# Kernel optimization log

Hardware: AMD Instinct MI355X
Metric: run time of the kernel (lower is better)

## Reference

```python
import jax, jax.numpy as jnp
import numpy as np

B, N, D_IN, D_OUT, H = 8, 1024, 768, 768, 12
D_HEAD = D_OUT // H  # 64; per-head softmax scale is sqrt(D_HEAD)


def setup_inputs() -> dict:
    key = jax.random.key(0)
    kx, kq, kk, kv, kwo, kbo = jax.random.split(key, 6)
    s_in = 1.0 / np.sqrt(D_IN)
    s_out = 1.0 / np.sqrt(D_OUT)
    return {
        "x": jax.random.normal(kx, (B, N, D_IN), dtype=jnp.float32),
        # stacked per-head Linear weights, torch layout [out, in] -> [H, d_head, D_IN]
        "Wq": jax.random.uniform(kq, (H, D_HEAD, D_IN), jnp.float32, -s_in, s_in),
        "Wk": jax.random.uniform(kk, (H, D_HEAD, D_IN), jnp.float32, -s_in, s_in),
        "Wv": jax.random.uniform(kv, (H, D_HEAD, D_IN), jnp.float32, -s_in, s_in),
        "Wo": jax.random.uniform(kwo, (D_OUT, D_OUT), jnp.float32, -s_out, s_out),
        "bo": jax.random.uniform(kbo, (D_OUT,), jnp.float32, -s_out, s_out),
    }


def reference(x, Wq, Wk, Wv, Wo, bo):
    # Per-head projections, batched over heads: [B, H, N, d_head]
    q = jnp.einsum('bnd,hed->bhne', x, Wq)
    k = jnp.einsum('bnd,hed->bhne', x, Wk)
    v = jnp.einsum('bnd,hed->bhne', x, Wv)
    scale = 1.0 / np.sqrt(D_HEAD)
    scores = jnp.einsum('bhie,bhje->bhij', q, k) * scale  # [B, H, N, N]
    att = jax.nn.softmax(scores, axis=-1)
    out = jnp.einsum('bhij,bhje->bhie', att, v)  # [B, H, N, d_head]
    # concat heads along last dim: [B, N, H*d_head]
    out = out.transpose(0, 2, 1, 3).reshape(B, N, D_OUT)
    return out @ Wo.T + bo
```

## Files before the change

kernel.cpp:

```cpp
#include <hip/hip_runtime.h>
#include <hip/hip_bf16.h>


typedef unsigned short u16;
typedef unsigned int u32;
typedef __attribute__((ext_vector_type(8))) short bf8;
typedef __attribute__((ext_vector_type(4))) short bf4;
typedef __attribute__((ext_vector_type(4))) float f4;
typedef __attribute__((ext_vector_type(4))) unsigned short us4;

#define NB 8
#define NSEQ 1024
#define DMODEL 768
#define NHEAD 12
#define DHEAD 64

#define XELEMS   (NB * NSEQ * DMODEL)
#define WELEMS   (DMODEL * DMODEL)

__device__ __forceinline__ float b2f(u16 u) {
  union { unsigned int i; float f; } c; c.i = ((unsigned int)u) << 16; return c.f;
}
__device__ __forceinline__ u16 f2b(float f) {
  union { float f; unsigned int i; } c; c.f = f;
  unsigned int r = c.i + 0x7fffu + ((c.i >> 16) & 1u);
  return (u16)(r >> 16);
}
__device__ __forceinline__ void gl_lds16(const u16* g, u16* l) {
  __builtin_amdgcn_global_load_lds(
      (const __attribute__((address_space(1))) unsigned int*)g,
      (__attribute__((address_space(3))) unsigned int*)l, 16, 0, 0);
}

struct CvtArgs {
  const float* src[5];
  u16* dst[5];
};
#define G0 (XELEMS / 4)
#define GW (WELEMS / 4)
#define GTOT (G0 + 4 * GW)

__global__ __launch_bounds__(256) void cvt_kernel(CvtArgs a) {
  size_t g = (size_t)blockIdx.x * 256 + threadIdx.x;
  if (g >= GTOT) return;
  int t; size_t off;
  if (g < G0) { t = 0; off = g; }
  else { size_t r = g - G0; t = 1 + (int)(r / GW); off = r % GW; }
  f4 v = *(const f4*)(a.src[t] + off * 4);
  us4 o;
  o[0] = f2b(v[0]); o[1] = f2b(v[1]); o[2] = f2b(v[2]); o[3] = f2b(v[3]);
  *(us4*)(a.dst[t] + off * 4) = o;
}

__global__ __launch_bounds__(512, 2) void qkv_gemm(
    const u16* __restrict__ x, const u16* __restrict__ Wq,
    const u16* __restrict__ Wk, const u16* __restrict__ Wv,
    u16* __restrict__ q, u16* __restrict__ k, u16* __restrict__ vt)
{
  __shared__ __align__(16) u16 lA[3][256 * 64];
  __shared__ __align__(16) u16 lB[3][128 * 64];

  const int tid  = threadIdx.x;
  const int lane = tid & 63;
  const int w    = tid >> 6;
  const int wm4  = w >> 1;
  const int wn2  = w & 1;
  const int col  = lane & 15;
  const int quad = lane >> 4;

  const int bid = blockIdx.x;
  const int xcd = bid & 7;
  const int j   = bid >> 3;
  const int bng = j / 24;
  const int bm4 = (j % 24) / 6;
  const int bn6 = j % 6;
  const int bm  = xcd * 4 + bm4;
  const int bn  = bng * 6 + bn6;

  const int m0 = bm * 256;
  const int proj = bn / 6;
  const u16* Wsel = (proj == 0) ? Wq : (proj == 1 ? Wk : Wv);
  const int nrem0 = (bn % 6) * 128;

  const int srow8 = lane >> 3;
  const int sg    = (lane & 7) ^ srow8;

  const u16* gA = x    + (size_t)(m0    + w * 8 + srow8) * DMODEL + sg * 8;
  const u16* gB = Wsel + (size_t)(nrem0 + w * 8 + srow8) * DMODEL + sg * 8;

  f4 acc[4][4];
#pragma unroll
  for (int i = 0; i < 4; i++)
#pragma unroll
    for (int jj = 0; jj < 4; jj++) acc[i][jj] = (f4)0.0f;

#define QKV_STAGE(T, BUF)                                                      \
  do {                                                                         \
    const int kk_ = (T) * 64;                                                  \
    _Pragma("unroll")                                                          \
    for (int r_ = 0; r_ < 4; r_++)                                             \
      gl_lds16(gA + (size_t)r_ * 64 * DMODEL + kk_,                            \
               &lA[BUF][(r_ * 64 + w * 8) * 64]);                              \
    _Pragma("unroll")                                                          \
    for (int r_ = 0; r_ < 2; r_++)                                             \
      gl_lds16(gB + (size_t)r_ * 64 * DMODEL + kk_,                            \
               &lB[BUF][(r_ * 64 + w * 8) * 64]);                              \
  } while (0)

  QKV_STAGE(0, 0);
  QKV_STAGE(1, 1);

  for (int t = 0; t < 12; t++) {
    if (t < 11) { asm volatile("s_waitcnt vmcnt(6)" ::: "memory"); }
    else        { asm volatile("s_waitcnt vmcnt(0)" ::: "memory"); }
    __builtin_amdgcn_s_barrier();
    asm volatile("" ::: "memory");

    if (t < 10) QKV_STAGE(t + 2, (t + 2) % 3);

    const int buf = t % 3;
    bf8 af[4][2], bfr[4][2];
#pragma unroll
    for (int mt = 0; mt < 4; mt++) {
      const int row = wm4 * 64 + mt * 16 + col;
#pragma unroll
      for (int kt = 0; kt < 2; kt++)
        af[mt][kt] = *(const bf8*)&lA[buf][row * 64 + (((kt * 4 + quad) ^ (row & 7)) << 3)];
    }
#pragma unroll
    for (int nt = 0; nt < 4; nt++) {
      const int row = wn2 * 64 + nt * 16 + col;
#pragma unroll
      for (int kt = 0; kt < 2; kt++)
        bfr[nt][kt] = *(const bf8*)&lB[buf][row * 64 + (((kt * 4 + quad) ^ (row & 7)) << 3)];
    }

    __builtin_amdgcn_s_setprio(1);
#pragma unroll
    for (int mt = 0; mt < 4; mt++)
#pragma unroll
      for (int nt = 0; nt < 4; nt++)
#pragma unroll
        for (int kt = 0; kt < 2; kt++)
          acc[mt][nt] = __builtin_amdgcn_mfma_f32_16x16x32_bf16(af[mt][kt], bfr[nt][kt], acc[mt][nt], 0, 0, 0);
    __builtin_amdgcn_s_setprio(0);
  }
#undef QKV_STAGE

  const int mw0 = m0 + wm4 * 64, nw0 = nrem0 + wn2 * 64;
  if (proj == 2) {
#pragma unroll
    for (int mt = 0; mt < 4; mt++) {
#pragma unroll
      for (int nt = 0; nt < 4; nt++) {
        const int nc = nw0 + nt * 16 + col;
        const int h = nc >> 6, e = nc & 63;
        const int t0 = mw0 + mt * 16 + quad * 4;
        const int b = t0 >> 10, tok0 = t0 & 1023;
        us4 pk;
#pragma unroll
        for (int r = 0; r < 4; r++) pk[r] = f2b(acc[mt][nt][r]);
        *(us4*)(vt + ((size_t)(b * NHEAD + h) * DHEAD + e) * NSEQ + tok0) = pk;
      }
    }
  } else {
    u16* dst = (proj == 0) ? q : k;
#pragma unroll
    for (int mt = 0; mt < 4; mt++) {
#pragma unroll
      for (int nt = 0; nt < 4; nt++) {
        const int nc = nw0 + nt * 16 + col;
        const int h = nc >> 6, e = nc & 63;
#pragma unroll
        for (int r = 0; r < 4; r++) {
          const int t = mw0 + mt * 16 + quad * 4 + r;
          const int b = t >> 10, tok = t & 1023;
          dst[((size_t)(b * NHEAD + h) * NSEQ + tok) * DHEAD + e] = f2b(acc[mt][nt][r]);
        }
      }
    }
  }
}

__global__ __launch_bounds__(256, 3) void attn_kernel(
    const u16* __restrict__ q, const u16* __restrict__ k,
    const u16* __restrict__ vt, u16* __restrict__ attn)
{
  __shared__ __align__(16) u16 ldsK[2][64 * 64];
  __shared__ __align__(16) u16 ldsV[2][64 * 64];
  __shared__ __align__(16) u16 ldsP[4][32][72];

  const int tid  = threadIdx.x;
  const int lane = tid & 63;
  const int w    = tid >> 6;
  const int col  = lane & 15;
  const int quad = lane >> 4;

  const int idx = blockIdx.x;
  const int bh = idx % 96, qc = idx / 96;
  const int b = bh / 12, h = bh % 12;

  const size_t head = ((size_t)b * NHEAD + h) * NSEQ * DHEAD;
  const int q0 = qc * 128 + w * 32;

  const int srow8 = lane >> 3;
  const int sg    = (lane & 7) ^ srow8;

  bf8 onesf;
#pragma unroll
  for (int jj = 0; jj < 8; jj++) onesf[jj] = (short)0x3F80;

  bf8 qf[2][2];
#pragma unroll
  for (int qt = 0; qt < 2; qt++)
#pragma unroll
    for (int kt = 0; kt < 2; kt++) {
      const int row = q0 + qt * 16 + col;
      bf8 t = *(const bf8*)(q + head + (size_t)row * DHEAD + kt * 32 + quad * 8);
#pragma unroll
      for (int jj = 0; jj < 8; jj++) t[jj] = (short)f2b(b2f((u16)t[jj]) * 0.125f);
      qf[qt][kt] = t;
    }

  f4 lacc[2];
  f4 o[2][4];
#pragma unroll
  for (int mt = 0; mt < 2; mt++) {
    lacc[mt] = (f4)0.0f;
#pragma unroll
    for (int et = 0; et < 4; et++) o[mt][et] = (f4)0.0f;
  }

#pragma unroll
  for (int i = 0; i < 2; i++) {
    const int li = w * 2 + i;
    gl_lds16(k  + head + (size_t)(li * 8 + srow8) * DHEAD + sg * 8, &ldsK[0][li * 512]);
    gl_lds16(vt + head + (size_t)(li * 8 + srow8) * NSEQ + sg * 8,  &ldsV[0][li * 512]);
  }

  for (int t = 0; t < NSEQ / 64; t++) {
    const int cur = t & 1;
    __syncthreads();
    if (t < NSEQ / 64 - 1) {
      const int kb2 = (t + 1) * 64;
#pragma unroll
      for (int i = 0; i < 2; i++) {
        const int li = w * 2 + i;
        gl_lds16(k  + head + (size_t)(kb2 + li * 8 + srow8) * DHEAD + sg * 8,
                 &ldsK[cur ^ 1][li * 512]);
        gl_lds16(vt + head + (size_t)(li * 8 + srow8) * NSEQ + kb2 + sg * 8,
                 &ldsV[cur ^ 1][li * 512]);
      }
    }

    f4 st[4][2];
#pragma unroll
    for (int kvt = 0; kvt < 4; kvt++)
#pragma unroll
      for (int qt = 0; qt < 2; qt++) st[kvt][qt] = (f4)0.0f;
#pragma unroll
    for (int kt = 0; kt < 2; kt++) {
      bf8 kf[4];
#pragma unroll
      for (int kvt = 0; kvt < 4; kvt++) {
        const int row = kvt * 16 + col;
        kf[kvt] = *(const bf8*)&ldsK[cur][row * 64 + (((kt * 4 + quad) ^ (col & 7)) << 3)];
      }
      __builtin_amdgcn_s_setprio(1);
#pragma unroll
      for (int kvt = 0; kvt < 4; kvt++)
#pragma unroll
        for (int qt = 0; qt < 2; qt++)
          st[kvt][qt] = __builtin_amdgcn_mfma_f32_16x16x32_bf16(kf[kvt], qf[qt][kt], st[kvt][qt], 0, 0, 0);
      __builtin_amdgcn_s_setprio(0);
    }

#pragma unroll
    for (int kvt = 0; kvt < 4; kvt++)
#pragma unroll
      for (int qt = 0; qt < 2; qt++) {
        const f4 p = st[kvt][qt];
        bf4 pw;
        pw[0] = (short)f2b(__expf(p[0]));
        pw[1] = (short)f2b(__expf(p[1]));
        pw[2] = (short)f2b(__expf(p[2]));
        pw[3] = (short)f2b(__expf(p[3]));
        *(bf4*)&ldsP[w][qt * 16 + col][kvt * 16 + quad * 4] = pw;
      }
    asm volatile("" ::: "memory");

#pragma unroll
    for (int kt2 = 0; kt2 < 2; kt2++) {
      bf8 vf[4];
#pragma unroll
      for (int et = 0; et < 4; et++) {
        const int row = et * 16 + col;
        vf[et] = *(const bf8*)&ldsV[cur][row * 64 + (((kt2 * 4 + quad) ^ (col & 7)) << 3)];
      }
#pragma unroll
      for (int mt = 0; mt < 2; mt++) {
        const bf8 pf = *(const bf8*)&ldsP[w][mt * 16 + col][kt2 * 32 + quad * 8];
        __builtin_amdgcn_s_setprio(1);
        lacc[mt] = __builtin_amdgcn_mfma_f32_16x16x32_bf16(pf, onesf, lacc[mt], 0, 0, 0);
#pragma unroll
        for (int et = 0; et < 4; et++)
          o[mt][et] = __builtin_amdgcn_mfma_f32_16x16x32_bf16(pf, vf[et], o[mt][et], 0, 0, 0);
        __builtin_amdgcn_s_setprio(0);
      }
    }
  }

#pragma unroll
  for (int mt = 0; mt < 2; mt++)
#pragma unroll
    for (int r = 0; r < 4; r++) {
      const float inv = 1.0f / lacc[mt][r];
      const int token = q0 + mt * 16 + quad * 4 + r;
#pragma unroll
      for (int et = 0; et < 4; et++)
        attn[(size_t)(b * NSEQ + token) * DMODEL + h * DHEAD + et * 16 + col] =
            f2b(o[mt][et][r] * inv);
    }
}

__global__ __launch_bounds__(256, 4) void out_gemm(
    const u16* __restrict__ attn, const u16* __restrict__ Wo,
    const float* __restrict__ bo, float* __restrict__ out)
{
  __shared__ __align__(16) u16 lA[2][128 * 32];
  __shared__ __align__(16) u16 lB[2][128 * 32];

  const int tid  = threadIdx.x;
  const int lane = tid & 63;
  const int w    = tid >> 6;
  const int wm   = w >> 1, wn = w & 1;
  const int col  = lane & 15;
  const int quad = lane >> 4;
  const int bm = blockIdx.x;
  const int bn = blockIdx.y;

  const int m0 = bm * 128;
  const int n0 = bn * 128;

  const int srow = lane >> 2;
  const int sg   = (lane & 3) ^ ((srow >> 1) & 3);
  const u16* gA0 = attn + (size_t)(m0 + w * 32 + srow) * DMODEL + sg * 8;
  const u16* gB0 = Wo   + (size_t)(n0 + w * 32 + srow) * DMODEL + sg * 8;

  f4 acc[4][4];
#pragma unroll
  for (int i = 0; i < 4; i++)
#pragma unroll
    for (int jj = 0; jj < 4; jj++) acc[i][jj] = (f4)0.0f;

  gl_lds16(gA0, &lA[0][(w * 32) * 32]);
  gl_lds16(gA0 + (size_t)16 * DMODEL, &lA[0][(w * 32 + 16) * 32]);
  gl_lds16(gB0, &lB[0][(w * 32) * 32]);
  gl_lds16(gB0 + (size_t)16 * DMODEL, &lB[0][(w * 32 + 16) * 32]);

  for (int it = 0; it < 24; it++) {
    const int cur = it & 1;
    __syncthreads();
    if (it < 23) {
      const int kk = (it + 1) * 32;
      gl_lds16(gA0 + kk, &lA[cur ^ 1][(w * 32) * 32]);
      gl_lds16(gA0 + (size_t)16 * DMODEL + kk, &lA[cur ^ 1][(w * 32 + 16) * 32]);
      gl_lds16(gB0 + kk, &lB[cur ^ 1][(w * 32) * 32]);
      gl_lds16(gB0 + (size_t)16 * DMODEL + kk, &lB[cur ^ 1][(w * 32 + 16) * 32]);
    }

    bf8 af[4], bfr[4];
#pragma unroll
    for (int mt = 0; mt < 4; mt++) {
      const int row = wm * 64 + mt * 16 + col;
      af[mt] = *(const bf8*)&lA[cur][row * 32 + ((quad ^ ((row >> 1) & 3)) << 3)];
    }
#pragma unroll
    for (int nt = 0; nt < 4; nt++) {
      const int row = wn * 64 + nt * 16 + col;
      bfr[nt] = *(const bf8*)&lB[cur][row * 32 + ((quad ^ ((row >> 1) & 3)) << 3)];
    }
#pragma unroll
    for (int mt = 0; mt < 4; mt++)
#pragma unroll
      for (int nt = 0; nt < 4; nt++)
        acc[mt][nt] = __builtin_amdgcn_mfma_f32_16x16x32_bf16(af[mt], bfr[nt], acc[mt][nt], 0, 0, 0);
  }

  const int mw0 = m0 + wm * 64, nw0 = n0 + wn * 64;
#pragma unroll
  for (int mt = 0; mt < 4; mt++)
#pragma unroll
    for (int nt = 0; nt < 4; nt++) {
      const int n = nw0 + nt * 16 + col;
      const float bias = bo[n];
#pragma unroll
      for (int r = 0; r < 4; r++) {
        const int row = mw0 + mt * 16 + quad * 4 + r;
        out[(size_t)row * DMODEL + n] = acc[mt][nt][r] + bias;
      }
    }
}

extern "C" void kernel_launch(void* const* d_in, const int* in_sizes, int n_in,
                              void* d_out, int out_size, void* d_ws, size_t ws_size,
                              hipStream_t stream) {
  const float* x  = (const float*)d_in[0];
  const float* Wq = (const float*)d_in[1];
  const float* Wk = (const float*)d_in[2];
  const float* Wv = (const float*)d_in[3];
  const float* Wo = (const float*)d_in[4];
  const float* bo = (const float*)d_in[5];
  float* out = (float*)d_out;

  u16* xb   = (u16*)d_ws;
  u16* wqb  = xb  + XELEMS;
  u16* wkb  = wqb + WELEMS;
  u16* wvb  = wkb + WELEMS;
  u16* wob  = wvb + WELEMS;
  u16* q    = wob + WELEMS;
  u16* k    = q   + XELEMS;
  u16* vt   = k   + XELEMS;
  u16* attn = vt  + XELEMS;

  CvtArgs ca;
  ca.src[0] = x;  ca.src[1] = Wq;  ca.src[2] = Wk;  ca.src[3] = Wv;  ca.src[4] = Wo;
  ca.dst[0] = xb; ca.dst[1] = wqb; ca.dst[2] = wkb; ca.dst[3] = wvb; ca.dst[4] = wob;

  cvt_kernel<<<dim3((GTOT + 255) / 256), 256, 0, stream>>>(ca);
  qkv_gemm<<<dim3(576), 512, 0, stream>>>(xb, wqb, wkb, wvb, q, k, vt);
  attn_kernel<<<dim3(768), 256, 0, stream>>>(q, k, vt, attn);
  out_gemm<<<dim3(64, 6), 256, 0, stream>>>(attn, wob, bo, out);
}
```

Measured before the change: 193.7 us.

## Replace double-buffered LDS DMA with register-staged single buffer in attention

The attention kernel stops using direct global-to-LDS loads into two K/V buffers. It now loads the next K/V tile into registers at the top of each iteration and writes it into a single LDS buffer after compute, guarded by two barriers. Halving K/V LDS use allows raising the occupancy hint from 3 to 4 blocks per CU. The cost is an extra barrier per iteration, more VGPRs for the staged tiles, and LDS stores that no longer overlap with compute.

```diff
diff --git a/kernel.cpp b/kernel.cpp
--- a/kernel.cpp
+++ b/kernel.cpp
@@ -182,12 +182,12 @@
   }
 }
 
-__global__ __launch_bounds__(256, 3) void attn_kernel(
+__global__ __launch_bounds__(256, 4) void attn_kernel(
     const u16* __restrict__ q, const u16* __restrict__ k,
     const u16* __restrict__ vt, u16* __restrict__ attn)
 {
-  __shared__ __align__(16) u16 ldsK[2][64 * 64];
-  __shared__ __align__(16) u16 ldsV[2][64 * 64];
+  __shared__ __align__(16) u16 ldsK[64 * 64];
+  __shared__ __align__(16) u16 ldsV[64 * 64];
   __shared__ __align__(16) u16 ldsP[4][32][72];
 
   const int tid  = threadIdx.x;
@@ -204,7 +204,18 @@
   const int q0 = qc * 128 + w * 32;
 
   const int srow8 = lane >> 3;
-  const int sg    = (lane & 7) ^ srow8;
+  const int lg    = lane & 7;
+  const int sg    = lg ^ srow8;
+
+  const int li0 = w * 2, li1 = w * 2 + 1;
+  const u16* ksrc0 = k  + head + (size_t)(li0 * 8 + srow8) * DHEAD + sg * 8;
+  const u16* ksrc1 = k  + head + (size_t)(li1 * 8 + srow8) * DHEAD + sg * 8;
+  const u16* vsrc0 = vt + head + (size_t)(li0 * 8 + srow8) * NSEQ + sg * 8;
+  const u16* vsrc1 = vt + head + (size_t)(li1 * 8 + srow8) * NSEQ + sg * 8;
+  u16* kdst0 = &ldsK[(li0 * 8 + srow8) * 64 + lg * 8];
+  u16* kdst1 = &ldsK[(li1 * 8 + srow8) * 64 + lg * 8];
+  u16* vdst0 = &ldsV[(li0 * 8 + srow8) * 64 + lg * 8];
+  u16* vdst1 = &ldsV[(li1 * 8 + srow8) * 64 + lg * 8];
 
   bf8 onesf;
 #pragma unroll
@@ -231,26 +242,24 @@
     for (int et = 0; et < 4; et++) o[mt][et] = (f4)0.0f;
   }
 
-#pragma unroll
-  for (int i = 0; i < 2; i++) {
-    const int li = w * 2 + i;
-    gl_lds16(k  + head + (size_t)(li * 8 + srow8) * DHEAD + sg * 8, &ldsK[0][li * 512]);
-    gl_lds16(vt + head + (size_t)(li * 8 + srow8) * NSEQ + sg * 8,  &ldsV[0][li * 512]);
-  }
+  {
+    bf8 k0 = *(const bf8*)ksrc0;
+    bf8 k1 = *(const bf8*)ksrc1;
+    bf8 v0 = *(const bf8*)vsrc0;
+    bf8 v1 = *(const bf8*)vsrc1;
+    *(bf8*)kdst0 = k0; *(bf8*)kdst1 = k1;
+    *(bf8*)vdst0 = v0; *(bf8*)vdst1 = v1;
+  }
+  __syncthreads();
 
   for (int t = 0; t < NSEQ / 64; t++) {
-    const int cur = t & 1;
-    __syncthreads();
+    bf8 nk0, nk1, nv0, nv1;
     if (t < NSEQ / 64 - 1) {
       const int kb2 = (t + 1) * 64;
-#pragma unroll
-      for (int i = 0; i < 2; i++) {
-        const int li = w * 2 + i;
-        gl_lds16(k  + head + (size_t)(kb2 + li * 8 + srow8) * DHEAD + sg * 8,
-                 &ldsK[cur ^ 1][li * 512]);
-        gl_lds16(vt + head + (size_t)(li * 8 + srow8) * NSEQ + kb2 + sg * 8,
-                 &ldsV[cur ^ 1][li * 512]);
-      }
+      nk0 = *(const bf8*)(ksrc0 + (size_t)kb2 * DHEAD);
+      nk1 = *(const bf8*)(ksrc1 + (size_t)kb2 * DHEAD);
+      nv0 = *(const bf8*)(vsrc0 + kb2);
+      nv1 = *(const bf8*)(vsrc1 + kb2);
     }
 
     f4 st[4][2];
@@ -264,7 +273,7 @@
 #pragma unroll
       for (int kvt = 0; kvt < 4; kvt++) {
         const int row = kvt * 16 + col;
-        kf[kvt] = *(const bf8*)&ldsK[cur][row * 64 + (((kt * 4 + quad) ^ (col & 7)) << 3)];
+        kf[kvt] = *(const bf8*)&ldsK[row * 64 + (((kt * 4 + quad) ^ (col & 7)) << 3)];
       }
       __builtin_amdgcn_s_setprio(1);
 #pragma unroll
@@ -295,7 +304,7 @@
 #pragma unroll
       for (int et = 0; et < 4; et++) {
         const int row = et * 16 + col;
-        vf[et] = *(const bf8*)&ldsV[cur][row * 64 + (((kt2 * 4 + quad) ^ (col & 7)) << 3)];
+        vf[et] = *(const bf8*)&ldsV[row * 64 + (((kt2 * 4 + quad) ^ (col & 7)) << 3)];
       }
 #pragma unroll
       for (int mt = 0; mt < 2; mt++) {
@@ -307,6 +316,13 @@
           o[mt][et] = __builtin_amdgcn_mfma_f32_16x16x32_bf16(pf, vf[et], o[mt][et], 0, 0, 0);
         __builtin_amdgcn_s_setprio(0);
       }
+    }
+
+    if (t < NSEQ / 64 - 1) {
+      __syncthreads();
+      *(bf8*)kdst0 = nk0; *(bf8*)kdst1 = nk1;
+      *(bf8*)vdst0 = nv0; *(bf8*)vdst1 = nv1;
+      __syncthreads();
     }
   }
 
```

Measured after the change: 211.6 us. 1.09x slower.

## Shrink QKV GEMM tiles to 128x128 with double-buffered LDS and more blocks

Applied to the files above, without the earlier changes.

Changes the QKV projection GEMM from 256x128 tiles with 512 threads and a triple-buffered async pipeline to 128x128 tiles with 256 threads and a double buffer synchronized by __syncthreads. The grid doubles to 1152 blocks so the work spreads more evenly over the CUs, and per-block LDS use drops. In exchange, operand reuse per tile is lower, so more global traffic is needed. The fine-grained vmcnt waits are replaced by full barriers, so load latency may be hidden less well.

```diff
diff --git a/kernel.cpp b/kernel.cpp
--- a/kernel.cpp
+++ b/kernel.cpp
@@ -52,32 +52,33 @@
   *(us4*)(a.dst[t] + off * 4) = o;
 }
 
-__global__ __launch_bounds__(512, 2) void qkv_gemm(
+__global__ __launch_bounds__(256, 2) void qkv_gemm(
     const u16* __restrict__ x, const u16* __restrict__ Wq,
     const u16* __restrict__ Wk, const u16* __restrict__ Wv,
     u16* __restrict__ q, u16* __restrict__ k, u16* __restrict__ vt)
 {
-  __shared__ __align__(16) u16 lA[3][256 * 64];
-  __shared__ __align__(16) u16 lB[3][128 * 64];
+  __shared__ __align__(16) u16 lA[2][128 * 64];
+  __shared__ __align__(16) u16 lB[2][128 * 64];
 
   const int tid  = threadIdx.x;
   const int lane = tid & 63;
   const int w    = tid >> 6;
-  const int wm4  = w >> 1;
-  const int wn2  = w & 1;
+  const int wm   = w >> 1;
+  const int wn   = w & 1;
   const int col  = lane & 15;
   const int quad = lane >> 4;
 
   const int bid = blockIdx.x;
   const int xcd = bid & 7;
   const int j   = bid >> 3;
-  const int bng = j / 24;
-  const int bm4 = (j % 24) / 6;
-  const int bn6 = j % 6;
-  const int bm  = xcd * 4 + bm4;
+  const int bng = j / 48;
+  const int rr  = j % 48;
+  const int bm8 = rr / 6;
+  const int bn6 = rr % 6;
+  const int bm  = xcd * 8 + bm8;
   const int bn  = bng * 6 + bn6;
 
-  const int m0 = bm * 256;
+  const int m0 = bm * 128;
   const int proj = bn / 6;
   const u16* Wsel = (proj == 0) ? Wq : (proj == 1 ? Wk : Wv);
   const int nrem0 = (bn % 6) * 128;
@@ -85,8 +86,8 @@
   const int srow8 = lane >> 3;
   const int sg    = (lane & 7) ^ srow8;
 
-  const u16* gA = x    + (size_t)(m0    + w * 8 + srow8) * DMODEL + sg * 8;
-  const u16* gB = Wsel + (size_t)(nrem0 + w * 8 + srow8) * DMODEL + sg * 8;
+  const u16* gA = x    + (size_t)(m0    + w * 32 + srow8) * DMODEL + sg * 8;
+  const u16* gB = Wsel + (size_t)(nrem0 + w * 32 + srow8) * DMODEL + sg * 8;
 
   f4 acc[4][4];
 #pragma unroll
@@ -98,41 +99,36 @@
   do {                                                                         \
     const int kk_ = (T) * 64;                                                  \
     _Pragma("unroll")                                                          \
-    for (int r_ = 0; r_ < 4; r_++)                                             \
-      gl_lds16(gA + (size_t)r_ * 64 * DMODEL + kk_,                            \
-               &lA[BUF][(r_ * 64 + w * 8) * 64]);                              \
+    for (int i_ = 0; i_ < 4; i_++)                                             \
+      gl_lds16(gA + (size_t)(i_ * 8) * DMODEL + kk_,                           \
+               &lA[BUF][(w * 32 + i_ * 8) * 64]);                              \
     _Pragma("unroll")                                                          \
-    for (int r_ = 0; r_ < 2; r_++)                                             \
-      gl_lds16(gB + (size_t)r_ * 64 * DMODEL + kk_,                            \
-               &lB[BUF][(r_ * 64 + w * 8) * 64]);                              \
+    for (int i_ = 0; i_ < 4; i_++)                                             \
+      gl_lds16(gB + (size_t)(i_ * 8) * DMODEL + kk_,                           \
+               &lB[BUF][(w * 32 + i_ * 8) * 64]);                              \
   } while (0)
 
   QKV_STAGE(0, 0);
-  QKV_STAGE(1, 1);
+  __syncthreads();
 
   for (int t = 0; t < 12; t++) {
-    if (t < 11) { asm volatile("s_waitcnt vmcnt(6)" ::: "memory"); }
-    else        { asm volatile("s_waitcnt vmcnt(0)" ::: "memory"); }
-    __builtin_amdgcn_s_barrier();
-    asm volatile("" ::: "memory");
-
-    if (t < 10) QKV_STAGE(t + 2, (t + 2) % 3);
-
-    const int buf = t % 3;
+    const int cur = t & 1;
+    if (t < 11) QKV_STAGE(t + 1, cur ^ 1);
+
     bf8 af[4][2], bfr[4][2];
 #pragma unroll
     for (int mt = 0; mt < 4; mt++) {
-      const int row = wm4 * 64 + mt * 16 + col;
+      const int row = wm * 64 + mt * 16 + col;
 #pragma unroll
       for (int kt = 0; kt < 2; kt++)
-        af[mt][kt] = *(const bf8*)&lA[buf][row * 64 + (((kt * 4 + quad) ^ (row & 7)) << 3)];
+        af[mt][kt] = *(const bf8*)&lA[cur][row * 64 + (((kt * 4 + quad) ^ (row & 7)) << 3)];
     }
 #pragma unroll
     for (int nt = 0; nt < 4; nt++) {
-      const int row = wn2 * 64 + nt * 16 + col;
+      const int row = wn * 64 + nt * 16 + col;
 #pragma unroll
       for (int kt = 0; kt < 2; kt++)
-        bfr[nt][kt] = *(const bf8*)&lB[buf][row * 64 + (((kt * 4 + quad) ^ (row & 7)) << 3)];
+        bfr[nt][kt] = *(const bf8*)&lB[cur][row * 64 + (((kt * 4 + quad) ^ (row & 7)) << 3)];
     }
 
     __builtin_amdgcn_s_setprio(1);
@@ -144,10 +140,12 @@
         for (int kt = 0; kt < 2; kt++)
           acc[mt][nt] = __builtin_amdgcn_mfma_f32_16x16x32_bf16(af[mt][kt], bfr[nt][kt], acc[mt][nt], 0, 0, 0);
     __builtin_amdgcn_s_setprio(0);
+
+    __syncthreads();
   }
 #undef QKV_STAGE
 
-  const int mw0 = m0 + wm4 * 64, nw0 = nrem0 + wn2 * 64;
+  const int mw0 = m0 + wm * 64, nw0 = nrem0 + wn * 64;
   if (proj == 2) {
 #pragma unroll
     for (int mt = 0; mt < 4; mt++) {
@@ -428,7 +426,7 @@
   ca.dst[0] = xb; ca.dst[1] = wqb; ca.dst[2] = wkb; ca.dst[3] = wvb; ca.dst[4] = wob;
 
   cvt_kernel<<<dim3((GTOT + 255) / 256), 256, 0, stream>>>(ca);
-  qkv_gemm<<<dim3(576), 512, 0, stream>>>(xb, wqb, wkb, wvb, q, k, vt);
+  qkv_gemm<<<dim3(1152), 256, 0, stream>>>(xb, wqb, wkb, wvb, q, k, vt);
   attn_kernel<<<dim3(768), 256, 0, stream>>>(q, k, vt, attn);
   out_gemm<<<dim3(64, 6), 256, 0, stream>>>(attn, wob, bo, out);
 }
```

Result: faster. 185.8 us (-4.1%).
